# Kernel optimization log

Hardware: AMD Instinct MI355X
Metric: run time of the kernel (lower is better)

The kernel has to match this reference:

```python
import jax, jax.numpy as jnp
import numpy as np

B, C, H, W = 16, 512, 64, 64
NH = 8  # num_heads


def setup_inputs() -> dict:
    key = jax.random.key(0)
    ks = jax.random.split(key, 7)
    s = 1.0 / np.sqrt(C)
    return {
        "x": jax.random.normal(ks[0], (B, C, H, W), dtype=jnp.float32),
        "wq": jax.random.normal(ks[1], (C, C), dtype=jnp.float32) * s,
        "bq": jax.random.normal(ks[2], (C,), dtype=jnp.float32) * 0.01,
        "wk": jax.random.normal(ks[3], (C, C), dtype=jnp.float32) * s,
        "bk": jax.random.normal(ks[4], (C,), dtype=jnp.float32) * 0.01,
        "wv": jax.random.normal(ks[5], (C, C), dtype=jnp.float32) * s,
        "bv": jax.random.normal(ks[6], (C,), dtype=jnp.float32) * 0.01,
    }


def reference(x, wq, bq, wk, bk, wv, bv):
    b, c_in, h, w = x.shape
    hd = c_in // NH  # head dim

    def conv1x1(wt, bias):
        # 1x1 conv == channel GEMM: (b,c,h,w) x (o,c) -> (b,o,h,w)
        y = jnp.einsum("bchw,oc->bohw", x, wt) + bias[None, :, None, None]
        # view(b, nh, hd, h, w).permute(0,1,3,4,2) -> (b, nh, h, w, hd)
        return y.reshape(b, NH, hd, h, w).transpose(0, 1, 3, 4, 2)

    q = conv1x1(wq, bq)
    k = conv1x1(wk, bk)
    v = conv1x1(wv, bv)

    # attention along the width axis, per (batch, head, row)
    energy = jnp.einsum("bnhqc,bnhkc->bnhqk", q, k)  # (b,nh,h,w,w)
    attn = jax.nn.softmax(energy, axis=-1)
    out = jnp.einsum("bnhqk,bnhkc->bnhqc", attn, v)  # (b,nh,h,w,hd)

    # permute(0,1,4,2,3) -> (b,nh,hd,h,w) -> view(b, C, h, w)
    out = out.transpose(0, 1, 4, 2, 3).reshape(b, c_in, h, w)
    return out + x
```

## Files before the change

### kernel.cpp

```cpp
#include <hip/hip_runtime.h>
#include <stdint.h>

#define B_   16
#define C_   512
#define H_   64
#define W_   64
#define NH_  8
#define HD_  64
#define HW_  4096

typedef __attribute__((ext_vector_type(8))) _Float16 f16x8;
typedef __attribute__((ext_vector_type(8))) unsigned short u16x8;
typedef __attribute__((ext_vector_type(4))) unsigned short u16x4;
typedef __attribute__((ext_vector_type(4))) float f32x4;

static __device__ __forceinline__ unsigned short f2h(float f) {
  _Float16 h = (_Float16)f;
  unsigned short u;
  __builtin_memcpy(&u, &h, 2);
  return u;
}

static __device__ __forceinline__ void gld_lds16(const void* g, void* l) {
  __builtin_amdgcn_global_load_lds((__attribute__((address_space(1))) void*)g,
                                   (__attribute__((address_space(3))) void*)l,
                                   16, 0, 0);
}

__global__ __launch_bounds__(256) void rcca_tr(const float* __restrict__ x,
                                               unsigned short* __restrict__ xT) {
  __shared__ float lT[64 * 65];
  const int bid = blockIdx.x;
  const int st = bid & 63;
  const int ct = (bid >> 6) & 7;
  const int b  = bid >> 9;
  const int t = threadIdx.x;
  const int hwl = t & 63;
  const int cl0 = (t >> 6) * 16;
  const float* src = x + ((size_t)(b * C_ + ct * 64 + cl0)) * HW_ + st * 64 + hwl;
#pragma unroll
  for (int jj = 0; jj < 16; ++jj)
    lT[(cl0 + jj) * 65 + hwl] = src[(size_t)jj * HW_];
  __syncthreads();
  const int hw2 = t >> 2;
  const int cc0 = (t & 3) * 16;
  u16x8 o0, o1;
#pragma unroll
  for (int u = 0; u < 8; ++u) {
    o0[u] = f2h(lT[(cc0 + u) * 65 + hw2]);
    o1[u] = f2h(lT[(cc0 + 8 + u) * 65 + hw2]);
  }
  unsigned short* dst = xT + ((size_t)b * HW_ + st * 64 + hw2) * C_ + ct * 64 + cc0;
  *(u16x8*)dst = o0;
  *(u16x8*)(dst + 8) = o1;
}

__global__ __launch_bounds__(256) void rcca_cvtw(const float* __restrict__ wq,
                                                 const float* __restrict__ wk,
                                                 const float* __restrict__ wv,
                                                 unsigned short* __restrict__ Wc) {
  const int i = blockIdx.x * 256 + threadIdx.x;
  const int e = i * 4;
  const float* w = (e < 262144) ? wq : (e < 524288) ? wk : wv;
  const int off = e & 262143;
  const float4 v = *(const float4*)(w + off);
  u16x4 p;
  p[0] = f2h(v.x); p[1] = f2h(v.y); p[2] = f2h(v.z); p[3] = f2h(v.w);
  *(u16x4*)(Wc + e) = p;
}

__global__ __launch_bounds__(256) void rcca_fused(
    const unsigned short* __restrict__ xT, const unsigned short* __restrict__ Wc,
    const float* __restrict__ bq, const float* __restrict__ bk, const float* __restrict__ bv,
    const float* __restrict__ x, float* __restrict__ out) {
  __shared__ __align__(16) char smem[73728];
  unsigned short* lA = (unsigned short*)smem;
  unsigned short* lB = (unsigned short*)(smem + 16384);
  const int sbid = blockIdx.x;
  const int lg = ((sbid & 7) << 9) | (sbid >> 3);
  const int head = lg & 7;
  const int bh = lg >> 3;
  const int b = bh >> 5;
  const int ht = bh & 31;
  const int t = threadIdx.x;
  const int wid = t >> 6, lane = t & 63, r = lane & 15, q = lane >> 4;
  const int rx = r & 7;
  const int wm = wid >> 1, wn = wid & 1;
  const int arow = t >> 3;
  const int acol = ((t & 7) ^ (arow & 7)) * 8;
  char* lAb = (char*)lA;
  char* lBb = (char*)lB;
  const int wbase = wid * 1024;
  const unsigned short* Abase = xT + ((size_t)b * HW_ + ht * 128) * C_;
  const unsigned short* Bbase = Wc + (size_t)head * 64 * C_;
  f32x4 acc[4][6];
#pragma unroll
  for (int i = 0; i < 4; ++i)
#pragma unroll
    for (int j = 0; j < 6; ++j) acc[i][j] = (f32x4){0.f, 0.f, 0.f, 0.f};

  for (int k0 = 0; k0 < C_; k0 += 64) {
    __syncthreads();
#pragma unroll
    for (int rr = 0; rr < 4; ++rr)
      gld_lds16(Abase + (size_t)(rr * 32 + arow) * C_ + k0 + acol, lAb + rr * 4096 + wbase);
#pragma unroll
    for (int p = 0; p < 6; ++p) {
      const size_t grow = (size_t)((p >> 1) * 512 + (p & 1) * 32 + arow) * C_;
      gld_lds16(Bbase + grow + k0 + acol, lBb + p * 4096 + wbase);
    }
    __syncthreads();
#pragma unroll
    for (int kk = 0; kk < 64; kk += 32) {
      const int cb = ((kk >> 3) + q) ^ rx;
      f16x8 av[4], bw[6];
#pragma unroll
      for (int i = 0; i < 4; ++i)
        av[i] = *(const f16x8*)&lA[(wm * 64 + i * 16 + r) * 64 + cb * 8];
#pragma unroll
      for (int j = 0; j < 6; ++j)
        bw[j] = *(const f16x8*)&lB[(wn * 96 + j * 16 + r) * 64 + cb * 8];
#pragma unroll
      for (int i = 0; i < 4; ++i)
#pragma unroll
        for (int j = 0; j < 6; ++j)
          acc[i][j] = __builtin_amdgcn_mfma_f32_16x16x32_f16(av[i], bw[j], acc[i][j], 0, 0, 0);
    }
  }
  __syncthreads();
  unsigned short* sQh = (unsigned short*)(smem + wm * 27648);
  unsigned short* sKh = (unsigned short*)(smem + wm * 27648 + 9216);
  unsigned short* sVh = (unsigned short*)(smem + wm * 27648 + 18432);
#pragma unroll
  for (int j = 0; j < 6; ++j) {
    const int n0 = wn * 96 + j * 16;
    const int sel = n0 >> 6;
    const int dd = (n0 & 63) + r;
    const float* bias = (sel == 0) ? bq : (sel == 1) ? bk : bv;
    const float bias_v = bias[head * 64 + dd];
    if (sel < 2) {
      unsigned short* dst = (sel == 0) ? sQh : sKh;
#pragma unroll
      for (int i = 0; i < 4; ++i)
#pragma unroll
        for (int reg = 0; reg < 4; ++reg)
          dst[(i * 16 + q * 4 + reg) * 72 + dd] = f2h(acc[i][j][reg] + bias_v);
    } else {
#pragma unroll
      for (int i = 0; i < 4; ++i) {
        u16x4 pk;
#pragma unroll
        for (int reg = 0; reg < 4; ++reg) pk[reg] = f2h(acc[i][j][reg] + bias_v);
        *(u16x4*)&sVh[dd * 72 + i * 16 + q * 4] = pk;
      }
    }
  }
  __syncthreads();
  unsigned short* sPh = (unsigned short*)(smem + 55296 + wm * 9216);
  f32x4 s2[2][4];
#pragma unroll
  for (int i2 = 0; i2 < 2; ++i2)
#pragma unroll
    for (int j = 0; j < 4; ++j) s2[i2][j] = (f32x4){0.f, 0.f, 0.f, 0.f};
#pragma unroll
  for (int kk = 0; kk < 64; kk += 32) {
    f16x8 aq0 = *(const f16x8*)&sQh[(wn * 32 + r) * 72 + kk + q * 8];
    f16x8 aq1 = *(const f16x8*)&sQh[(wn * 32 + 16 + r) * 72 + kk + q * 8];
#pragma unroll
    for (int j = 0; j < 4; ++j) {
      f16x8 bk8 = *(const f16x8*)&sKh[(j * 16 + r) * 72 + kk + q * 8];
      s2[0][j] = __builtin_amdgcn_mfma_f32_16x16x32_f16(aq0, bk8, s2[0][j], 0, 0, 0);
      s2[1][j] = __builtin_amdgcn_mfma_f32_16x16x32_f16(aq1, bk8, s2[1][j], 0, 0, 0);
    }
  }
  float inv2[2][4];
#pragma unroll
  for (int i2 = 0; i2 < 2; ++i2)
#pragma unroll
    for (int reg = 0; reg < 4; ++reg) {
      float mx = fmaxf(fmaxf(s2[i2][0][reg], s2[i2][1][reg]),
                       fmaxf(s2[i2][2][reg], s2[i2][3][reg]));
#pragma unroll
      for (int o = 1; o < 16; o <<= 1) mx = fmaxf(mx, __shfl_xor(mx, o, 64));
      float p0 = __expf(s2[i2][0][reg] - mx);
      float p1 = __expf(s2[i2][1][reg] - mx);
      float p2 = __expf(s2[i2][2][reg] - mx);
      float p3 = __expf(s2[i2][3][reg] - mx);
      float sum = p0 + p1 + p2 + p3;
#pragma unroll
      for (int o = 1; o < 16; o <<= 1) sum += __shfl_xor(sum, o, 64);
      inv2[i2][reg] = 1.0f / sum;
      const int row = wn * 32 + i2 * 16 + q * 4 + reg;
      sPh[row * 72 + r] = f2h(p0);
      sPh[row * 72 + 16 + r] = f2h(p1);
      sPh[row * 72 + 32 + r] = f2h(p2);
      sPh[row * 72 + 48 + r] = f2h(p3);
    }
  __syncthreads();
  f32x4 o4[2][4];
#pragma unroll
  for (int i2 = 0; i2 < 2; ++i2)
#pragma unroll
    for (int jd = 0; jd < 4; ++jd) o4[i2][jd] = (f32x4){0.f, 0.f, 0.f, 0.f};
#pragma unroll
  for (int kk = 0; kk < 64; kk += 32) {
    f16x8 ap0 = *(const f16x8*)&sPh[(wn * 32 + r) * 72 + kk + q * 8];
    f16x8 ap1 = *(const f16x8*)&sPh[(wn * 32 + 16 + r) * 72 + kk + q * 8];
#pragma unroll
    for (int jd = 0; jd < 4; ++jd) {
      f16x8 bv8 = *(const f16x8*)&sVh[(jd * 16 + r) * 72 + kk + q * 8];
      o4[0][jd] = __builtin_amdgcn_mfma_f32_16x16x32_f16(ap0, bv8, o4[0][jd], 0, 0, 0);
      o4[1][jd] = __builtin_amdgcn_mfma_f32_16x16x32_f16(ap1, bv8, o4[1][jd], 0, 0, 0);
    }
  }
  float* sOh = (float*)(smem + wm * 27648);
#pragma unroll
  for (int i2 = 0; i2 < 2; ++i2)
#pragma unroll
    for (int jd = 0; jd < 4; ++jd) {
      const int d = jd * 16 + r;
#pragma unroll
      for (int reg = 0; reg < 4; ++reg) {
        const int w = wn * 32 + i2 * 16 + q * 4 + reg;
        sOh[d * 66 + w] = o4[i2][jd][reg] * inv2[i2][reg];
      }
    }
  __syncthreads();
  const int d = t >> 2, w0 = (t & 3) * 16;
#pragma unroll
  for (int hs = 0; hs < 2; ++hs) {
    const float* sO2 = (const float*)(smem + hs * 27648);
    const int h = ht * 2 + hs;
    const size_t obase = (((size_t)b * C_ + head * 64 + d) * H_ + h) * (size_t)W_ + w0;
    const float4* xr = (const float4*)(x + obase);
    float4* op = (float4*)(out + obase);
#pragma unroll
    for (int u = 0; u < 4; ++u) {
      float4 xv = xr[u];
      float4 ov;
      ov.x = sO2[d * 66 + w0 + u * 4 + 0] + xv.x;
      ov.y = sO2[d * 66 + w0 + u * 4 + 1] + xv.y;
      ov.z = sO2[d * 66 + w0 + u * 4 + 2] + xv.z;
      ov.w = sO2[d * 66 + w0 + u * 4 + 3] + xv.w;
      op[u] = ov;
    }
  }
}

extern "C" void kernel_launch(void* const* d_in, const int* in_sizes, int n_in,
                              void* d_out, int out_size, void* d_ws, size_t ws_size,
                              hipStream_t stream) {
  const float* x  = (const float*)d_in[0];
  const float* wq = (const float*)d_in[1];
  const float* bq = (const float*)d_in[2];
  const float* wk = (const float*)d_in[3];
  const float* bk = (const float*)d_in[4];
  const float* wv = (const float*)d_in[5];
  const float* bv = (const float*)d_in[6];
  float* out = (float*)d_out;
  char* ws = (char*)d_ws;
  unsigned short* xT = (unsigned short*)ws;
  unsigned short* Wc = (unsigned short*)(ws + (size_t)67108864);
  hipLaunchKernelGGL(rcca_tr,    dim3(8192), dim3(256), 0, stream, x, xT);
  hipLaunchKernelGGL(rcca_cvtw,  dim3(768),  dim3(256), 0, stream, wq, wk, wv, Wc);
  hipLaunchKernelGGL(rcca_fused, dim3(4096), dim3(256), 0, stream, xT, Wc, bq, bk, bv, x, out);
}
```

Baseline: 422.9 us.

## Fuse x transpose and fp16 conversion into the fused GEMM-attention kernel

Removes the separate transpose kernel that wrote an fp16 channel-last copy of x to workspace. The fused kernel now loads fp32 x tiles directly into LDS, then converts and transposes them into the swizzled fp16 A tile before the MFMA loop. This drops a full read and write pass over x and one launch. In exchange each block reads fp32 (twice the bytes of fp16), and every k-step gets an extra LDS pass and barrier. The x tile is re-read by all 8 head blocks, which relies on cache hits.

```diff
diff --git a/kernel.cpp b/kernel.cpp
--- a/kernel.cpp
+++ b/kernel.cpp
@@ -25,34 +25,6 @@
   __builtin_amdgcn_global_load_lds((__attribute__((address_space(1))) void*)g,
                                    (__attribute__((address_space(3))) void*)l,
                                    16, 0, 0);
-}
-
-__global__ __launch_bounds__(256) void rcca_tr(const float* __restrict__ x,
-                                               unsigned short* __restrict__ xT) {
-  __shared__ float lT[64 * 65];
-  const int bid = blockIdx.x;
-  const int st = bid & 63;
-  const int ct = (bid >> 6) & 7;
-  const int b  = bid >> 9;
-  const int t = threadIdx.x;
-  const int hwl = t & 63;
-  const int cl0 = (t >> 6) * 16;
-  const float* src = x + ((size_t)(b * C_ + ct * 64 + cl0)) * HW_ + st * 64 + hwl;
-#pragma unroll
-  for (int jj = 0; jj < 16; ++jj)
-    lT[(cl0 + jj) * 65 + hwl] = src[(size_t)jj * HW_];
-  __syncthreads();
-  const int hw2 = t >> 2;
-  const int cc0 = (t & 3) * 16;
-  u16x8 o0, o1;
-#pragma unroll
-  for (int u = 0; u < 8; ++u) {
-    o0[u] = f2h(lT[(cc0 + u) * 65 + hw2]);
-    o1[u] = f2h(lT[(cc0 + 8 + u) * 65 + hw2]);
-  }
-  unsigned short* dst = xT + ((size_t)b * HW_ + st * 64 + hw2) * C_ + ct * 64 + cc0;
-  *(u16x8*)dst = o0;
-  *(u16x8*)(dst + 8) = o1;
 }
 
 __global__ __launch_bounds__(256) void rcca_cvtw(const float* __restrict__ wq,
@@ -70,12 +42,13 @@
 }
 
 __global__ __launch_bounds__(256) void rcca_fused(
-    const unsigned short* __restrict__ xT, const unsigned short* __restrict__ Wc,
+    const float* __restrict__ x, const unsigned short* __restrict__ Wc,
     const float* __restrict__ bq, const float* __restrict__ bk, const float* __restrict__ bv,
-    const float* __restrict__ x, float* __restrict__ out) {
+    float* __restrict__ out) {
   __shared__ __align__(16) char smem[73728];
   unsigned short* lA = (unsigned short*)smem;
   unsigned short* lB = (unsigned short*)(smem + 16384);
+  float* sX = (float*)(smem + 40960);
   const int sbid = blockIdx.x;
   const int lg = ((sbid & 7) << 9) | (sbid >> 3);
   const int head = lg & 7;
@@ -88,11 +61,14 @@
   const int wm = wid >> 1, wn = wid & 1;
   const int arow = t >> 3;
   const int acol = ((t & 7) ^ (arow & 7)) * 8;
-  char* lAb = (char*)lA;
   char* lBb = (char*)lB;
+  char* sXb = (char*)sX;
   const int wbase = wid * 1024;
-  const unsigned short* Abase = xT + ((size_t)b * HW_ + ht * 128) * C_;
+  const int xc = t >> 5;
+  const int xch = t & 31;
+  const float* Xbase = x + (size_t)b * C_ * HW_ + (size_t)ht * 128;
   const unsigned short* Bbase = Wc + (size_t)head * 64 * C_;
+  const int thw = t >> 1, thalf = t & 1;
   f32x4 acc[4][6];
 #pragma unroll
   for (int i = 0; i < 4; ++i)
@@ -102,12 +78,24 @@
   for (int k0 = 0; k0 < C_; k0 += 64) {
     __syncthreads();
 #pragma unroll
-    for (int rr = 0; rr < 4; ++rr)
-      gld_lds16(Abase + (size_t)(rr * 32 + arow) * C_ + k0 + acol, lAb + rr * 4096 + wbase);
+    for (int rr = 0; rr < 8; ++rr) {
+      const int c = rr * 8 + xc;
+      gld_lds16(Xbase + (size_t)(k0 + c) * HW_ + xch * 4, sXb + rr * 4096 + wbase);
+    }
 #pragma unroll
     for (int p = 0; p < 6; ++p) {
       const size_t grow = (size_t)((p >> 1) * 512 + (p & 1) * 32 + arow) * C_;
       gld_lds16(Bbase + grow + k0 + acol, lBb + p * 4096 + wbase);
+    }
+    __syncthreads();
+#pragma unroll
+    for (int u = 0; u < 4; ++u) {
+      const int chunk = thalf * 4 + u;
+      u16x8 pk;
+#pragma unroll
+      for (int j = 0; j < 8; ++j)
+        pk[j] = f2h(sX[(chunk * 8 + j) * 128 + thw]);
+      *(u16x8*)&lA[thw * 64 + ((chunk ^ (thw & 7)) * 8)] = pk;
     }
     __syncthreads();
 #pragma unroll
@@ -259,9 +247,7 @@
   const float* bv = (const float*)d_in[6];
   float* out = (float*)d_out;
   char* ws = (char*)d_ws;
-  unsigned short* xT = (unsigned short*)ws;
-  unsigned short* Wc = (unsigned short*)(ws + (size_t)67108864);
-  hipLaunchKernelGGL(rcca_tr,    dim3(8192), dim3(256), 0, stream, x, xT);
+  unsigned short* Wc = (unsigned short*)ws;
   hipLaunchKernelGGL(rcca_cvtw,  dim3(768),  dim3(256), 0, stream, wq, wk, wv, Wc);
-  hipLaunchKernelGGL(rcca_fused, dim3(4096), dim3(256), 0, stream, xT, Wc, bq, bk, bv, x, out);
-}
+  hipLaunchKernelGGL(rcca_fused, dim3(4096), dim3(256), 0, stream, x, Wc, bq, bk, bv, out);
+}
```

New measurement: 425.3 us. No clear change (+0.6%).

## Double-buffer the QKV projection k-loop with async LDS prefetch

Applied to the files above, without the earlier changes.

Splits the GEMM shared-memory staging into two buffers and unrolls the k-loop. Each iteration issues the global→LDS loads for the next 64-wide K slice before running the MFMAs on the current one, with a single barrier per iteration instead of two. This aims to hide global load latency behind matrix compute. The cost is more LDS per block (80KB instead of 72KB), which could limit how many blocks fit per CU.

```diff
diff --git a/kernel.cpp b/kernel.cpp
--- a/kernel.cpp
+++ b/kernel.cpp
@@ -73,9 +73,7 @@
     const unsigned short* __restrict__ xT, const unsigned short* __restrict__ Wc,
     const float* __restrict__ bq, const float* __restrict__ bk, const float* __restrict__ bv,
     const float* __restrict__ x, float* __restrict__ out) {
-  __shared__ __align__(16) char smem[73728];
-  unsigned short* lA = (unsigned short*)smem;
-  unsigned short* lB = (unsigned short*)(smem + 16384);
+  __shared__ __align__(16) char smem[81920];
   const int sbid = blockIdx.x;
   const int lg = ((sbid & 7) << 9) | (sbid >> 3);
   const int head = lg & 7;
@@ -87,9 +85,7 @@
   const int rx = r & 7;
   const int wm = wid >> 1, wn = wid & 1;
   const int arow = t >> 3;
-  const int acol = ((t & 7) ^ (arow & 7)) * 8;
-  char* lAb = (char*)lA;
-  char* lBb = (char*)lB;
+  const int acol = (((t & 7) ^ ((t >> 3) & 7)) * 8);
   const int wbase = wid * 1024;
   const unsigned short* Abase = xT + ((size_t)b * HW_ + ht * 128) * C_;
   const unsigned short* Bbase = Wc + (size_t)head * 64 * C_;
@@ -99,17 +95,38 @@
 #pragma unroll
     for (int j = 0; j < 6; ++j) acc[i][j] = (f32x4){0.f, 0.f, 0.f, 0.f};
 
-  for (int k0 = 0; k0 < C_; k0 += 64) {
-    __syncthreads();
+  {
+    char* lAb = smem;
+    char* lBb = smem + 16384;
 #pragma unroll
     for (int rr = 0; rr < 4; ++rr)
-      gld_lds16(Abase + (size_t)(rr * 32 + arow) * C_ + k0 + acol, lAb + rr * 4096 + wbase);
+      gld_lds16(Abase + (size_t)(rr * 32 + arow) * C_ + acol, lAb + rr * 4096 + wbase);
 #pragma unroll
     for (int p = 0; p < 6; ++p) {
       const size_t grow = (size_t)((p >> 1) * 512 + (p & 1) * 32 + arow) * C_;
-      gld_lds16(Bbase + grow + k0 + acol, lBb + p * 4096 + wbase);
-    }
-    __syncthreads();
+      gld_lds16(Bbase + grow + acol, lBb + p * 4096 + wbase);
+    }
+  }
+  __syncthreads();
+
+#pragma unroll
+  for (int tt = 0; tt < 8; ++tt) {
+    const int cur = tt & 1;
+    if (tt < 7) {
+      const int k0n = (tt + 1) * 64;
+      char* lAn = smem + (cur ^ 1) * 40960;
+      char* lBn = lAn + 16384;
+#pragma unroll
+      for (int rr = 0; rr < 4; ++rr)
+        gld_lds16(Abase + (size_t)(rr * 32 + arow) * C_ + k0n + acol, lAn + rr * 4096 + wbase);
+#pragma unroll
+      for (int p = 0; p < 6; ++p) {
+        const size_t grow = (size_t)((p >> 1) * 512 + (p & 1) * 32 + arow) * C_;
+        gld_lds16(Bbase + grow + k0n + acol, lBn + p * 4096 + wbase);
+      }
+    }
+    const unsigned short* lA = (const unsigned short*)(smem + cur * 40960);
+    const unsigned short* lB = (const unsigned short*)(smem + cur * 40960 + 16384);
 #pragma unroll
     for (int kk = 0; kk < 64; kk += 32) {
       const int cb = ((kk >> 3) + q) ^ rx;
@@ -126,8 +143,8 @@
         for (int j = 0; j < 6; ++j)
           acc[i][j] = __builtin_amdgcn_mfma_f32_16x16x32_f16(av[i], bw[j], acc[i][j], 0, 0, 0);
     }
-  }
-  __syncthreads();
+    __syncthreads();
+  }
   unsigned short* sQh = (unsigned short*)(smem + wm * 27648);
   unsigned short* sKh = (unsigned short*)(smem + wm * 27648 + 9216);
   unsigned short* sVh = (unsigned short*)(smem + wm * 27648 + 18432);
```

Result: slower. 469.9 us (+11.1%).

## Double-buffer the QKV projection GEMM K-loop with 32-wide LDS stages

Applied to the files above, without the earlier changes.

Replaces the single-buffered 64-wide K-tile loop with a two-stage LDS ping-pong of 32-wide K tiles, so global_load_lds for the next tile is issued before the MFMAs on the current one. It also changes the XOR swizzle to a 4-chunk pattern and drops one barrier per iteration. This is meant to hide global load latency behind compute. The cost is more loop iterations, each doing less MFMA work, plus a larger LDS footprint that stays within the existing 72KB allocation.

```diff
diff --git a/kernel.cpp b/kernel.cpp
--- a/kernel.cpp
+++ b/kernel.cpp
@@ -74,8 +74,6 @@
     const float* __restrict__ bq, const float* __restrict__ bk, const float* __restrict__ bv,
     const float* __restrict__ x, float* __restrict__ out) {
   __shared__ __align__(16) char smem[73728];
-  unsigned short* lA = (unsigned short*)smem;
-  unsigned short* lB = (unsigned short*)(smem + 16384);
   const int sbid = blockIdx.x;
   const int lg = ((sbid & 7) << 9) | (sbid >> 3);
   const int head = lg & 7;
@@ -84,50 +82,58 @@
   const int ht = bh & 31;
   const int t = threadIdx.x;
   const int wid = t >> 6, lane = t & 63, r = lane & 15, q = lane >> 4;
-  const int rx = r & 7;
   const int wm = wid >> 1, wn = wid & 1;
-  const int arow = t >> 3;
-  const int acol = ((t & 7) ^ (arow & 7)) * 8;
-  char* lAb = (char*)lA;
-  char* lBb = (char*)lB;
   const int wbase = wid * 1024;
   const unsigned short* Abase = xT + ((size_t)b * HW_ + ht * 128) * C_;
-  const unsigned short* Bbase = Wc + (size_t)head * 64 * C_;
   f32x4 acc[4][6];
 #pragma unroll
   for (int i = 0; i < 4; ++i)
 #pragma unroll
     for (int j = 0; j < 6; ++j) acc[i][j] = (f32x4){0.f, 0.f, 0.f, 0.f};
 
-  for (int k0 = 0; k0 < C_; k0 += 64) {
+  auto stage = [&](char* buf, int k0) {
+    char* lAb = buf;
+    char* lBb = buf + 8192;
+#pragma unroll
+    for (int rr = 0; rr < 2; ++rr) {
+      const int idx = rr * 256 + t;
+      const int row = idx >> 2, ch = idx & 3;
+      gld_lds16(Abase + (size_t)row * C_ + k0 + ((ch ^ (row & 3)) * 8),
+                lAb + rr * 4096 + wbase);
+    }
+#pragma unroll
+    for (int rr = 0; rr < 3; ++rr) {
+      const int idx = rr * 256 + t;
+      const int row = idx >> 2, ch = idx & 3;
+      const int wrow = (row >> 6) * 512 + head * 64 + (row & 63);
+      gld_lds16(Wc + (size_t)wrow * C_ + k0 + ((ch ^ (row & 3)) * 8),
+                lBb + rr * 4096 + wbase);
+    }
+  };
+
+  stage(smem, 0);
+  __syncthreads();
+
+  for (int tt = 0; tt < 16; ++tt) {
+    char* cur = smem + (tt & 1) * 20480;
+    if (tt < 15) stage(smem + ((tt & 1) ^ 1) * 20480, (tt + 1) * 32);
+    const unsigned short* lA = (const unsigned short*)cur;
+    const unsigned short* lB = (const unsigned short*)(cur + 8192);
+    const int cb = q ^ (r & 3);
+    f16x8 av[4], bw[6];
+#pragma unroll
+    for (int i = 0; i < 4; ++i)
+      av[i] = *(const f16x8*)&lA[(wm * 64 + i * 16 + r) * 32 + cb * 8];
+#pragma unroll
+    for (int j = 0; j < 6; ++j)
+      bw[j] = *(const f16x8*)&lB[(wn * 96 + j * 16 + r) * 32 + cb * 8];
+#pragma unroll
+    for (int i = 0; i < 4; ++i)
+#pragma unroll
+      for (int j = 0; j < 6; ++j)
+        acc[i][j] = __builtin_amdgcn_mfma_f32_16x16x32_f16(av[i], bw[j], acc[i][j], 0, 0, 0);
     __syncthreads();
-#pragma unroll
-    for (int rr = 0; rr < 4; ++rr)
-      gld_lds16(Abase + (size_t)(rr * 32 + arow) * C_ + k0 + acol, lAb + rr * 4096 + wbase);
-#pragma unroll
-    for (int p = 0; p < 6; ++p) {
-      const size_t grow = (size_t)((p >> 1) * 512 + (p & 1) * 32 + arow) * C_;
-      gld_lds16(Bbase + grow + k0 + acol, lBb + p * 4096 + wbase);
-    }
-    __syncthreads();
-#pragma unroll
-    for (int kk = 0; kk < 64; kk += 32) {
-      const int cb = ((kk >> 3) + q) ^ rx;
-      f16x8 av[4], bw[6];
-#pragma unroll
-      for (int i = 0; i < 4; ++i)
-        av[i] = *(const f16x8*)&lA[(wm * 64 + i * 16 + r) * 64 + cb * 8];
-#pragma unroll
-      for (int j = 0; j < 6; ++j)
-        bw[j] = *(const f16x8*)&lB[(wn * 96 + j * 16 + r) * 64 + cb * 8];
-#pragma unroll
-      for (int i = 0; i < 4; ++i)
-#pragma unroll
-        for (int j = 0; j < 6; ++j)
-          acc[i][j] = __builtin_amdgcn_mfma_f32_16x16x32_f16(av[i], bw[j], acc[i][j], 0, 0, 0);
-    }
-  }
-  __syncthreads();
+  }
   unsigned short* sQh = (unsigned short*)(smem + wm * 27648);
   unsigned short* sKh = (unsigned short*)(smem + wm * 27648 + 9216);
   unsigned short* sVh = (unsigned short*)(smem + wm * 27648 + 18432);
```

Result: slower. 494.7 us (+17.0%).
